# Performance work log

Measured on AMD Instinct MI355X. Metric: run time of the kernel, lower is better.

The kernel has to match this reference:

```python
import jax, jax.numpy as jnp
import numpy as np

DIM = 384; HEADS = 12; WS = 7; SHIFT = 3
IMG_H = 56; IMG_W = 56; B = 32; MLP_HID = 1536
N = WS * WS; HEAD_DIM = DIM // HEADS


def _rel_pos_index():
    # standard Swin relative position index, shape [N, N], values in [0, (2*WS-1)^2)
    coords = np.stack(np.meshgrid(np.arange(WS), np.arange(WS), indexing='ij')).reshape(2, -1)
    rel = (coords[:, :, None] - coords[:, None, :]).transpose(1, 2, 0)
    rel[..., 0] += WS - 1
    rel[..., 1] += WS - 1
    rel[..., 0] *= 2 * WS - 1
    return jnp.asarray(rel.sum(-1))

REL_IDX = _rel_pos_index()


def _shift_mask():
    # Swin shifted-window attention mask: 0 within region, -100 across regions
    img = np.zeros((IMG_H, IMG_W))
    cnt = 0
    for hs in (slice(0, -WS), slice(-WS, -SHIFT), slice(-SHIFT, None)):
        for ws_ in (slice(0, -WS), slice(-WS, -SHIFT), slice(-SHIFT, None)):
            img[hs, ws_] = cnt
            cnt += 1
    mw = img.reshape(IMG_H // WS, WS, IMG_W // WS, WS).transpose(0, 2, 1, 3).reshape(-1, N)
    am = mw[:, None, :] - mw[:, :, None]
    return jnp.asarray(np.where(am != 0, -100.0, 0.0).astype(np.float32))


def setup_inputs() -> dict:
    key = jax.random.key(0)
    ks = jax.random.split(key, 8)
    rn = lambda k, s: jax.random.normal(k, s, jnp.float32) * 0.02
    return {
        'x': jax.random.normal(ks[0], (B, IMG_H * IMG_W, DIM), jnp.float32),
        'mask': _shift_mask(),
        'w_ln1': jnp.ones((DIM,), jnp.float32), 'b_ln1': jnp.zeros((DIM,), jnp.float32),
        'w_qkv': rn(ks[1], (3 * DIM, DIM)), 'b_qkv': jnp.zeros((3 * DIM,), jnp.float32),
        'rel_bias': rn(ks[2], ((2 * WS - 1) ** 2, HEADS)),
        'w_proj': rn(ks[3], (DIM, DIM)), 'b_proj': jnp.zeros((DIM,), jnp.float32),
        'w_ln2': jnp.ones((DIM,), jnp.float32), 'b_ln2': jnp.zeros((DIM,), jnp.float32),
        'w_fc1': rn(ks[4], (MLP_HID, DIM)), 'b_fc1': jnp.zeros((MLP_HID,), jnp.float32),
        'w_fc2': rn(ks[5], (DIM, MLP_HID)), 'b_fc2': jnp.zeros((DIM,), jnp.float32),
        'H': IMG_H, 'W': IMG_W,
    }


def _ln(x, g, b, eps=1e-5):
    mu = x.mean(-1, keepdims=True)
    var = ((x - mu) ** 2).mean(-1, keepdims=True)
    return (x - mu) * jax.lax.rsqrt(var + eps) * g + b


def reference(x, mask, w_ln1, b_ln1, w_qkv, b_qkv, rel_bias, w_proj, b_proj,
              w_ln2, b_ln2, w_fc1, b_fc1, w_fc2, b_fc2, H, W):
    Bsz, L, C = x.shape
    nW = (H // WS) * (W // WS)
    shortcut = x
    h = _ln(x, w_ln1, b_ln1).reshape(Bsz, H, W, C)
    # cyclic shift
    h = jnp.roll(h, (-SHIFT, -SHIFT), axis=(1, 2))
    # window partition -> [B*nW, N, C]
    h = h.reshape(Bsz, H // WS, WS, W // WS, WS, C).transpose(0, 1, 3, 2, 4, 5).reshape(-1, N, C)
    nB = h.shape[0]
    qkv = (h @ w_qkv.T + b_qkv).reshape(nB, N, 3, HEADS, HEAD_DIM).transpose(2, 0, 3, 1, 4)
    q, k, v = qkv[0] * (HEAD_DIM ** -0.5), qkv[1], qkv[2]  # each [nB, heads, N, hd]
    attn = jnp.einsum('bhnd,bhmd->bhnm', q, k)
    bias = rel_bias[REL_IDX].transpose(2, 0, 1)  # [heads, N, N]
    attn = attn + bias[None]
    attn = attn.reshape(Bsz, nW, HEADS, N, N) + mask[None, :, None]
    attn = jax.nn.softmax(attn, axis=-1).reshape(nB, HEADS, N, N)
    o = jnp.einsum('bhnm,bhmd->bhnd', attn, v).transpose(0, 2, 1, 3).reshape(nB, N, C)
    o = o @ w_proj.T + b_proj
    # window reverse
    o = o.reshape(Bsz, H // WS, W // WS, WS, WS, C).transpose(0, 1, 3, 2, 4, 5).reshape(Bsz, H, W, C)
    o = jnp.roll(o, (SHIFT, SHIFT), axis=(1, 2)).reshape(Bsz, H * W, C)
    x = shortcut + o
    h2 = _ln(x, w_ln2, b_ln2)
    h2 = jax.nn.gelu(h2 @ w_fc1.T + b_fc1) @ w_fc2.T + b_fc2
    return x + h2
```

## Files before the change

### kernel.cpp

```cpp
#include <hip/hip_runtime.h>
#include <stdint.h>

#define B_     32
#define IMG    56
#define L_     (IMG*IMG)
#define C_     384
#define HEADS_ 12
#define HD     32
#define WS_    7
#define N_     49
#define NWIN   64
#define NB     (B_*NWIN)
#define M_TOK  (NB*N_)
#define QKVF   1152

typedef __attribute__((ext_vector_type(8))) short bf16x8;
typedef __attribute__((ext_vector_type(4))) float f32x4;
typedef __attribute__((ext_vector_type(4))) unsigned short u16x4;

__device__ __forceinline__ float bf2f(unsigned short u) {
  union { unsigned int u; float f; } c; c.u = ((unsigned int)u) << 16; return c.f;
}
__device__ __forceinline__ unsigned short f2bf(float f) {
  union { float f; unsigned int u; } c; c.f = f;
  unsigned int r = c.u + 0x7FFFu + ((c.u >> 16) & 1u);
  return (unsigned short)(r >> 16);
}

__device__ __forceinline__ void gload_lds16(const void* g, void* l) {
  __builtin_amdgcn_global_load_lds(
      (const __attribute__((address_space(1))) unsigned int*)(uintptr_t)g,
      (__attribute__((address_space(3))) unsigned int*)(uintptr_t)l,
      16, 0, 0);
}

#define MFMA16(a, b, c) __builtin_amdgcn_mfma_f32_16x16x32_bf16((a), (b), (c), 0, 0, 0)

__global__ __launch_bounds__(256) void k_prep(
    const float* __restrict__ w_qkv, const float* __restrict__ w_proj,
    const float* __restrict__ w_fc1, const float* __restrict__ w_fc2,
    const float* __restrict__ relb,  const float* __restrict__ mask,
    ushort* __restrict__ wbq, ushort* __restrict__ wbp,
    ushort* __restrict__ wb1, ushort* __restrict__ wb2,
    ushort* __restrict__ bm)
{
  int g = blockIdx.x * 256 + threadIdx.x;
  if (g < 442368)        { wbq[g]            = f2bf(w_qkv[g]); return; }
  if (g < 589824)        { wbp[g - 442368]   = f2bf(w_proj[g - 442368]); return; }
  if (g < 1179648)       { wb1[g - 589824]   = f2bf(w_fc1[g - 589824]); return; }
  if (g < 1769472)       { wb2[g - 1179648]  = f2bf(w_fc2[g - 1179648]); return; }
  int n = g - 1769472;
  int r    = n & 3;
  int col  = (n >> 2) & 63;
  int quad = (n >> 8) & 3;
  int i    = (n >> 10) & 3;
  int hw   = n >> 12;
  int h = hw % HEADS_, wc = hw / HEADS_;
  int row = i * 16 + quad * 4 + r;
  float v;
  if (col >= N_) v = -30000.f;
  else if (row >= N_) v = 0.f;
  else {
    int idx = (row / WS_ - col / WS_ + 6) * 13 + (row % WS_ - col % WS_ + 6);
    v = relb[idx * HEADS_ + h] + mask[((size_t)wc * N_ + row) * N_ + col];
  }
  bm[n] = f2bf(v);
}

template<bool WINDOW>
__global__ __launch_bounds__(256) void k_ln(const float* __restrict__ X,
    const float* __restrict__ G, const float* __restrict__ Bb,
    ushort* __restrict__ out)
{
  int token = blockIdx.x * 4 + (threadIdx.x >> 6);
  int lane  = threadIdx.x & 63;
  const float* xp = X + (size_t)token * C_;
  float v[6];
#pragma unroll
  for (int t = 0; t < 6; t++) v[t] = xp[lane + 64*t];
  float s = 0.f, s2 = 0.f;
#pragma unroll
  for (int t = 0; t < 6; t++) { s += v[t]; s2 += v[t]*v[t]; }
#pragma unroll
  for (int off = 32; off > 0; off >>= 1) {
    s  += __shfl_down(s,  off, 64);
    s2 += __shfl_down(s2, off, 64);
  }
  s = __shfl(s, 0, 64); s2 = __shfl(s2, 0, 64);
  float mu   = s * (1.f / C_);
  float rstd = rsqrtf(s2 * (1.f / C_) - mu * mu + 1e-5f);
  size_t obase;
  if (WINDOW) {
    int b = token / L_, pix = token % L_;
    int hi = pix / IMG, wj = pix % IMG;
    int sh = hi - 3; if (sh < 0) sh += IMG;
    int sw = wj - 3; if (sw < 0) sw += IMG;
    int w = b * NWIN + (sh / WS_) * 8 + (sw / WS_);
    int p = (sh % WS_) * WS_ + (sw % WS_);
    obase = ((size_t)w * N_ + p) * C_;
  } else {
    obase = (size_t)token * C_;
  }
#pragma unroll
  for (int t = 0; t < 6; t++) {
    int c = lane + 64*t;
    out[obase + c] = f2bf((v[t] - mu) * rstd * G[c] + Bb[c]);
  }
}

template<int EPI, typename OutT>
__global__ __launch_bounds__(256, 2) void k_gemm(
    const ushort* __restrict__ A, const ushort* __restrict__ W,
    const float* __restrict__ bias, OutT* __restrict__ out,
    const float* __restrict__ res, int M, int N, int K)
{
  __shared__ __align__(16) ushort As[2][256*32];
  __shared__ __align__(16) ushort Bs[2][128*32];
  int ntn = N >> 7;
  int nwg = gridDim.x;
  int bid = (blockIdx.x & 7) * (nwg >> 3) + (blockIdx.x >> 3);
  int m0 = (bid / ntn) << 8;
  int n0 = (bid % ntn) << 7;
  int tid  = threadIdx.x;
  int wave = tid >> 6, lane = tid & 63;
  int l15  = lane & 15, quad = lane >> 4;
  int wm = (wave >> 1) << 7;
  int wn = (wave & 1) << 6;

  int srow = tid >> 2;
  int scol = (tid & 3) * 8;
  const ushort* gA = A + (size_t)(m0 + srow) * K + scol;
  const ushort* gB = W + (size_t)(n0 + srow) * K + scol;
  int oA = srow * 32 + scol;

  f32x4 acc[8][4];
#pragma unroll
  for (int i = 0; i < 8; i++)
#pragma unroll
    for (int j = 0; j < 4; j++) acc[i][j] = (f32x4){0.f, 0.f, 0.f, 0.f};

#pragma unroll
  for (int it = 0; it < 4; it++)
    gload_lds16(gA + (size_t)it * 64 * K, &As[0][oA + it * 2048]);
#pragma unroll
  for (int it = 0; it < 2; it++)
    gload_lds16(gB + (size_t)it * 64 * K, &Bs[0][oA + it * 2048]);
  gA += 32; gB += 32;
  asm volatile("s_waitcnt vmcnt(0)" : : : "memory");
  __syncthreads();

  int nt = K >> 5;
  int cur = 0;
  for (int t = 0; t < nt; t++) {
    int nxt = cur ^ 1;
    if (t + 1 < nt) {
#pragma unroll
      for (int it = 0; it < 4; it++)
        gload_lds16(gA + (size_t)it * 64 * K, &As[nxt][oA + it * 2048]);
#pragma unroll
      for (int it = 0; it < 2; it++)
        gload_lds16(gB + (size_t)it * 64 * K, &Bs[nxt][oA + it * 2048]);
      gA += 32; gB += 32;
    }
    bf16x8 af[8], bfr[4];
#pragma unroll
    for (int i = 0; i < 8; i++) af[i]  = *(const bf16x8*)&As[cur][(wm + i*16 + l15)*32 + quad*8];
#pragma unroll
    for (int j = 0; j < 4; j++) bfr[j] = *(const bf16x8*)&Bs[cur][(wn + j*16 + l15)*32 + quad*8];
#pragma unroll
    for (int i = 0; i < 8; i++)
#pragma unroll
      for (int j = 0; j < 4; j++)
        acc[i][j] = MFMA16(af[i], bfr[j], acc[i][j]);
    asm volatile("s_waitcnt vmcnt(0)" : : : "memory");
    __syncthreads();
    cur = nxt;
  }

  float bv[4];
#pragma unroll
  for (int j = 0; j < 4; j++) bv[j] = bias[n0 + wn + j*16 + l15];
#pragma unroll
  for (int i = 0; i < 8; i++) {
#pragma unroll
    for (int r = 0; r < 4; r++) {
      int row = m0 + wm + i*16 + quad*4 + r;
      size_t dstbase;
      if (EPI == 1) {
        int w = row / N_, p = row % N_;
        int b = w >> 6, wi = w & 63;
        int hi = (wi >> 3) * WS_ + p / WS_ + 3; if (hi >= IMG) hi -= IMG;
        int wj = (wi & 7)  * WS_ + p % WS_ + 3; if (wj >= IMG) wj -= IMG;
        dstbase = ((size_t)b * L_ + hi * IMG + wj) * C_;
      } else {
        dstbase = (size_t)row * N;
      }
#pragma unroll
      for (int j = 0; j < 4; j++) {
        int col = n0 + wn + j*16 + l15;
        float v = acc[i][j][r] + bv[j];
        if (EPI == 2) {
          float e = __expf(-1.5957691216057308f * (v + 0.044715f * v * v * v));
          v = v * __builtin_amdgcn_rcpf(1.f + e);
        }
        size_t dst = dstbase + col;
        if (EPI == 1) v += res[dst];
        if (EPI == 3) v += res[(size_t)row * N + col];
        if constexpr (sizeof(OutT) == 4) out[dst] = v;
        else                             out[dst] = f2bf(v);
      }
    }
  }
}

__global__ __launch_bounds__(256, 3) void k_attn_mfma(
    const ushort* __restrict__ qkv, const ushort* __restrict__ bm,
    ushort* __restrict__ out)
{
  __shared__ __align__(16) ushort Ps[4][64*64];
  __shared__ __align__(16) ushort Vt[4][32*64];
  int wave = threadIdx.x >> 6, lane = threadIdx.x & 63;
  int task = blockIdx.x * 4 + wave;
  int w = task / HEADS_, h = task % HEADS_;
  int l15 = lane & 15, quad = lane >> 4;

  const ushort* base = qkv + (size_t)w * N_ * QKVF + h * HD;

  bf16x8 qf[4], kf[4];
#pragma unroll
  for (int i = 0; i < 4; i++) {
    int rr = i * 16 + l15; if (rr > 48) rr = 48;
    const ushort* rp = base + (size_t)rr * QKVF + quad * 8;
    qf[i] = *(const bf16x8*)rp;
    kf[i] = *(const bf16x8*)(rp + C_);
  }

  {
    int m = lane > 48 ? 48 : lane;
    const ushort* vp = base + (size_t)m * QKVF + 2 * C_;
    bf16x8 v0 = *(const bf16x8*)vp;
    bf16x8 v1 = *(const bf16x8*)(vp + 8);
    bf16x8 v2 = *(const bf16x8*)(vp + 16);
    bf16x8 v3 = *(const bf16x8*)(vp + 24);
    ushort* vt = &Vt[wave][0];
#pragma unroll
    for (int d = 0; d < 32; d++) {
      ushort val = (ushort)(d < 8 ? v0[d & 7] : d < 16 ? v1[d & 7]
                                  : d < 24 ? v2[d & 7] : v3[d & 7]);
      vt[d * 64 + (lane ^ ((d & 7) << 3))] = val;
    }
  }

  f32x4 acc[4][4];
#pragma unroll
  for (int i = 0; i < 4; i++)
#pragma unroll
    for (int j = 0; j < 4; j++) acc[i][j] = (f32x4){0.f, 0.f, 0.f, 0.f};
#pragma unroll
  for (int i = 0; i < 4; i++)
#pragma unroll
    for (int j = 0; j < 4; j++)
      acc[i][j] = MFMA16(qf[i], kf[j], acc[i][j]);

  const ushort* bmb = bm + ((size_t)(w & 63) * HEADS_ + h) * 4096;
  float sv[4][4][4];
#pragma unroll
  for (int i = 0; i < 4; i++)
#pragma unroll
    for (int j = 0; j < 4; j++) {
      u16x4 bv = *(const u16x4*)(bmb + (((i * 4 + quad) * 64) + (j * 16 + l15)) * 4);
#pragma unroll
      for (int r = 0; r < 4; r++)
        sv[i][j][r] = acc[i][j][r] * 0.17677669529663687f + bf2f(bv[r]);
    }

  float mx[4][4], sm[4][4];
#pragma unroll
  for (int i = 0; i < 4; i++)
#pragma unroll
    for (int r = 0; r < 4; r++)
      mx[i][r] = fmaxf(fmaxf(sv[i][0][r], sv[i][1][r]),
                       fmaxf(sv[i][2][r], sv[i][3][r]));
#pragma unroll
  for (int off = 1; off <= 8; off <<= 1)
#pragma unroll
    for (int i = 0; i < 4; i++)
#pragma unroll
      for (int r = 0; r < 4; r++)
        mx[i][r] = fmaxf(mx[i][r], __shfl_xor(mx[i][r], off, 64));
#pragma unroll
  for (int i = 0; i < 4; i++)
#pragma unroll
    for (int r = 0; r < 4; r++) sm[i][r] = 0.f;
#pragma unroll
  for (int i = 0; i < 4; i++)
#pragma unroll
    for (int j = 0; j < 4; j++)
#pragma unroll
      for (int r = 0; r < 4; r++) {
        float e = __expf(sv[i][j][r] - mx[i][r]);
        sv[i][j][r] = e;
        sm[i][r] += e;
      }
#pragma unroll
  for (int off = 1; off <= 8; off <<= 1)
#pragma unroll
    for (int i = 0; i < 4; i++)
#pragma unroll
      for (int r = 0; r < 4; r++)
        sm[i][r] += __shfl_xor(sm[i][r], off, 64);

  ushort* pw = &Ps[wave][0];
#pragma unroll
  for (int i = 0; i < 4; i++)
#pragma unroll
    for (int r = 0; r < 4; r++) {
      float inv = __builtin_amdgcn_rcpf(sm[i][r]);
      int row = i * 16 + quad * 4 + r;
      int s = (row & 7) << 3;
#pragma unroll
      for (int j = 0; j < 4; j++)
        pw[row * 64 + ((j * 16 + l15) ^ s)] = f2bf(sv[i][j][r] * inv);
    }

  f32x4 o[4][2];
#pragma unroll
  for (int i = 0; i < 4; i++)
#pragma unroll
    for (int jv = 0; jv < 2; jv++) o[i][jv] = (f32x4){0.f, 0.f, 0.f, 0.f};
  const ushort* vt = &Vt[wave][0];
#pragma unroll
  for (int ks = 0; ks < 2; ks++) {
    int kc = ks * 32 + quad * 8;
    bf16x8 pa[4], vb[2];
#pragma unroll
    for (int i = 0; i < 4; i++) {
      int row = i * 16 + l15;
      pa[i] = *(const bf16x8*)&pw[row * 64 + (kc ^ ((row & 7) << 3))];
    }
#pragma unroll
    for (int jv = 0; jv < 2; jv++) {
      int nn = jv * 16 + l15;
      vb[jv] = *(const bf16x8*)&vt[nn * 64 + (kc ^ ((nn & 7) << 3))];
    }
#pragma unroll
    for (int i = 0; i < 4; i++)
#pragma unroll
      for (int jv = 0; jv < 2; jv++)
        o[i][jv] = MFMA16(pa[i], vb[jv], o[i][jv]);
  }

  ushort* op = out + ((size_t)w * N_) * C_ + h * HD;
#pragma unroll
  for (int i = 0; i < 4; i++)
#pragma unroll
    for (int r = 0; r < 4; r++) {
      int row = i * 16 + quad * 4 + r;
      if (row < N_) {
#pragma unroll
        for (int jv = 0; jv < 2; jv++)
          op[(size_t)row * C_ + jv * 16 + l15] = f2bf(o[i][jv][r]);
      }
    }
}

extern "C" void kernel_launch(void* const* d_in, const int* in_sizes, int n_in,
                              void* d_out, int out_size, void* d_ws, size_t ws_size,
                              hipStream_t stream) {
  (void)in_sizes; (void)n_in; (void)out_size; (void)ws_size;
  const float* x      = (const float*)d_in[0];
  const float* mask   = (const float*)d_in[1];
  const float* w_ln1  = (const float*)d_in[2];
  const float* b_ln1  = (const float*)d_in[3];
  const float* w_qkv  = (const float*)d_in[4];
  const float* b_qkv  = (const float*)d_in[5];
  const float* relb   = (const float*)d_in[6];
  const float* w_proj = (const float*)d_in[7];
  const float* b_proj = (const float*)d_in[8];
  const float* w_ln2  = (const float*)d_in[9];
  const float* b_ln2  = (const float*)d_in[10];
  const float* w_fc1  = (const float*)d_in[11];
  const float* b_fc1  = (const float*)d_in[12];
  const float* w_fc2  = (const float*)d_in[13];
  const float* b_fc2  = (const float*)d_in[14];

  char* ws = (char*)d_ws;
  ushort* r0 = (ushort*)ws;
  ushort* r1 = (ushort*)(ws + 308281344);
  ushort* bmt = (ushort*)(ws + 231211008);
  ushort* wbq = (ushort*)(ws + 385351680);
  ushort* wbp = wbq + QKVF * C_;
  ushort* wb1 = wbp + C_ * C_;
  ushort* wb2 = wb1 + 1536 * C_;
  float*  x1   = (float*)d_out;
  float*  outp = (float*)d_out;

  k_prep<<<4915200/256, 256, 0, stream>>>(w_qkv, w_proj, w_fc1, w_fc2,
                                          relb, mask, wbq, wbp, wb1, wb2, bmt);

  k_ln<true ><<<M_TOK/4, 256, 0, stream>>>(x, w_ln1, b_ln1, r1);
  k_gemm<0, ushort><<<(M_TOK/256)*(QKVF/128), 256, 0, stream>>>(
      r1, wbq, b_qkv, r0, nullptr, M_TOK, QKVF, 384);
  k_attn_mfma<<<NB*HEADS_/4, 256, 0, stream>>>(r0, bmt, r1);
  k_gemm<1, float><<<(M_TOK/256)*(C_/128), 256, 0, stream>>>(
      r1, wbp, b_proj, x1, x, M_TOK, C_, 384);
  k_ln<false><<<M_TOK/4, 256, 0, stream>>>(x1, w_ln2, b_ln2, r1);
  k_gemm<2, ushort><<<(M_TOK/256)*(1536/128), 256, 0, stream>>>(
      r1, wb1, b_fc1, r0, nullptr, M_TOK, 1536, 384);
  k_gemm<3, float><<<(M_TOK/256)*(C_/128), 256, 0, stream>>>(
      r0, wb2, b_fc2, outp, x1, M_TOK, C_, 1536);
}
```

Measured before the change: 1.004 ms.

## Rewrite GEMM as 8-wave kernel with triple-buffered BK=64 LDS pipeline

Replaces the 4-wave double-buffered GEMM with an 8-wave (512-thread) kernel. Each wave now owns a 64x64 tile, and the kernel uses K-tiles of 64 with three LDS stages. The A/B tiles are stored in XOR-swizzled LDS to avoid bank conflicts. Global-to-LDS prefetch is split across two half-iterations, and the MFMA blocks run under raised s_setprio with partial vmcnt waits, so loads overlap compute. LDS use grows to 144KB per block, which limits occupancy to one block per CU, and the barrier-heavy schedule must be correct for every K.

Result: slower. 1.054 ms (+5.0%).

```diff
diff --git a/kernel.cpp b/kernel.cpp
--- a/kernel.cpp
+++ b/kernel.cpp
@@ -109,13 +109,13 @@
 }
 
 template<int EPI, typename OutT>
-__global__ __launch_bounds__(256, 2) void k_gemm(
+__global__ __launch_bounds__(512) void k_gemm8(
     const ushort* __restrict__ A, const ushort* __restrict__ W,
     const float* __restrict__ bias, OutT* __restrict__ out,
     const float* __restrict__ res, int M, int N, int K)
 {
-  __shared__ __align__(16) ushort As[2][256*32];
-  __shared__ __align__(16) ushort Bs[2][128*32];
+  __shared__ __align__(16) ushort As[3][256*64];
+  __shared__ __align__(16) ushort Bs[3][128*64];
   int ntn = N >> 7;
   int nwg = gridDim.x;
   int bid = (blockIdx.x & 7) * (nwg >> 3) + (blockIdx.x >> 3);
@@ -124,64 +124,101 @@
   int tid  = threadIdx.x;
   int wave = tid >> 6, lane = tid & 63;
   int l15  = lane & 15, quad = lane >> 4;
-  int wm = (wave >> 1) << 7;
+  int wm = (wave >> 1) << 6;
   int wn = (wave & 1) << 6;
 
-  int srow = tid >> 2;
-  int scol = (tid & 3) * 8;
-  const ushort* gA = A + (size_t)(m0 + srow) * K + scol;
-  const ushort* gB = W + (size_t)(n0 + srow) * K + scol;
-  int oA = srow * 32 + scol;
-
-  f32x4 acc[8][4];
-#pragma unroll
-  for (int i = 0; i < 8; i++)
+  int srow = (wave << 3) + (lane >> 3);
+  int lgsw = (lane & 7) ^ ((lane >> 3) & 7);
+  const ushort* gAs = A + (size_t)(m0 + srow) * K + lgsw * 8;
+  const ushort* gBs = W + (size_t)(n0 + srow) * K + lgsw * 8;
+  int oL = (wave << 9) + (lane << 3);
+
+  int pg0 = quad ^ (l15 & 7);
+
+  f32x4 acc[4][4];
+#pragma unroll
+  for (int i = 0; i < 4; i++)
 #pragma unroll
     for (int j = 0; j < 4; j++) acc[i][j] = (f32x4){0.f, 0.f, 0.f, 0.f};
 
 #pragma unroll
-  for (int it = 0; it < 4; it++)
-    gload_lds16(gA + (size_t)it * 64 * K, &As[0][oA + it * 2048]);
-#pragma unroll
-  for (int it = 0; it < 2; it++)
-    gload_lds16(gB + (size_t)it * 64 * K, &Bs[0][oA + it * 2048]);
-  gA += 32; gB += 32;
-  asm volatile("s_waitcnt vmcnt(0)" : : : "memory");
-  __syncthreads();
-
-  int nt = K >> 5;
-  int cur = 0;
+  for (int tt = 0; tt < 2; tt++) {
+#pragma unroll
+    for (int ro = 0; ro < 4; ro++)
+      gload_lds16(gAs + (size_t)(ro * 64) * K + tt * 64, &As[tt][ro * 4096 + oL]);
+#pragma unroll
+    for (int ro = 0; ro < 2; ro++)
+      gload_lds16(gBs + (size_t)(ro * 64) * K + tt * 64, &Bs[tt][ro * 4096 + oL]);
+  }
+  asm volatile("s_waitcnt vmcnt(6)" ::: "memory");
+  __builtin_amdgcn_s_barrier();
+
+  int nt = K >> 6;
+  int rd = 0, wr = 2;
+  int kcol = 128;
   for (int t = 0; t < nt; t++) {
-    int nxt = cur ^ 1;
-    if (t + 1 < nt) {
-#pragma unroll
-      for (int it = 0; it < 4; it++)
-        gload_lds16(gA + (size_t)it * 64 * K, &As[nxt][oA + it * 2048]);
-#pragma unroll
-      for (int it = 0; it < 2; it++)
-        gload_lds16(gB + (size_t)it * 64 * K, &Bs[nxt][oA + it * 2048]);
-      gA += 32; gB += 32;
-    }
-    bf16x8 af[8], bfr[4];
-#pragma unroll
-    for (int i = 0; i < 8; i++) af[i]  = *(const bf16x8*)&As[cur][(wm + i*16 + l15)*32 + quad*8];
-#pragma unroll
-    for (int j = 0; j < 4; j++) bfr[j] = *(const bf16x8*)&Bs[cur][(wn + j*16 + l15)*32 + quad*8];
-#pragma unroll
-    for (int i = 0; i < 8; i++)
+    bool pre = (t + 2 < nt);
+    const ushort* as = &As[0][0] + rd * 16384;
+    const ushort* bs = &Bs[0][0] + rd * 8192;
+
+    bf16x8 af[4], bfr[4];
+#pragma unroll
+    for (int i = 0; i < 4; i++)
+      af[i]  = *(const bf16x8*)&as[(wm + i*16 + l15) * 64 + pg0 * 8];
+#pragma unroll
+    for (int j = 0; j < 4; j++)
+      bfr[j] = *(const bf16x8*)&bs[(wn + j*16 + l15) * 64 + pg0 * 8];
+    if (pre) {
+#pragma unroll
+      for (int ro = 0; ro < 3; ro++)
+        gload_lds16(gAs + (size_t)(ro * 64) * K + kcol, &As[wr][ro * 4096 + oL]);
+    }
+    __builtin_amdgcn_s_barrier();
+    __builtin_amdgcn_s_setprio(1);
+#pragma unroll
+    for (int i = 0; i < 4; i++)
 #pragma unroll
       for (int j = 0; j < 4; j++)
         acc[i][j] = MFMA16(af[i], bfr[j], acc[i][j]);
-    asm volatile("s_waitcnt vmcnt(0)" : : : "memory");
-    __syncthreads();
-    cur = nxt;
+    __builtin_amdgcn_s_setprio(0);
+    __builtin_amdgcn_s_barrier();
+
+#pragma unroll
+    for (int i = 0; i < 4; i++)
+      af[i]  = *(const bf16x8*)&as[(wm + i*16 + l15) * 64 + (pg0 ^ 4) * 8];
+#pragma unroll
+    for (int j = 0; j < 4; j++)
+      bfr[j] = *(const bf16x8*)&bs[(wn + j*16 + l15) * 64 + (pg0 ^ 4) * 8];
+    if (pre) {
+      gload_lds16(gAs + (size_t)(3 * 64) * K + kcol, &As[wr][3 * 4096 + oL]);
+#pragma unroll
+      for (int ro = 0; ro < 2; ro++)
+        gload_lds16(gBs + (size_t)(ro * 64) * K + kcol, &Bs[wr][ro * 4096 + oL]);
+      kcol += 64;
+    }
+    __builtin_amdgcn_s_barrier();
+    __builtin_amdgcn_s_setprio(1);
+#pragma unroll
+    for (int i = 0; i < 4; i++)
+#pragma unroll
+      for (int j = 0; j < 4; j++)
+        acc[i][j] = MFMA16(af[i], bfr[j], acc[i][j]);
+    __builtin_amdgcn_s_setprio(0);
+
+    if (t + 1 < nt) {
+      if (pre) asm volatile("s_waitcnt vmcnt(6)" ::: "memory");
+      else     asm volatile("s_waitcnt vmcnt(0)" ::: "memory");
+    }
+    __builtin_amdgcn_s_barrier();
+    rd = (rd == 2) ? 0 : rd + 1;
+    wr = (wr == 2) ? 0 : wr + 1;
   }
 
   float bv[4];
 #pragma unroll
   for (int j = 0; j < 4; j++) bv[j] = bias[n0 + wn + j*16 + l15];
 #pragma unroll
-  for (int i = 0; i < 8; i++) {
+  for (int i = 0; i < 4; i++) {
 #pragma unroll
     for (int r = 0; r < 4; r++) {
       int row = m0 + wm + i*16 + quad*4 + r;
@@ -399,14 +436,14 @@
                                           relb, mask, wbq, wbp, wb1, wb2, bmt);
 
   k_ln<true ><<<M_TOK/4, 256, 0, stream>>>(x, w_ln1, b_ln1, r1);
-  k_gemm<0, ushort><<<(M_TOK/256)*(QKVF/128), 256, 0, stream>>>(
+  k_gemm8<0, ushort><<<(M_TOK/256)*(QKVF/128), 512, 0, stream>>>(
       r1, wbq, b_qkv, r0, nullptr, M_TOK, QKVF, 384);
   k_attn_mfma<<<NB*HEADS_/4, 256, 0, stream>>>(r0, bmt, r1);
-  k_gemm<1, float><<<(M_TOK/256)*(C_/128), 256, 0, stream>>>(
+  k_gemm8<1, float><<<(M_TOK/256)*(C_/128), 512, 0, stream>>>(
       r1, wbp, b_proj, x1, x, M_TOK, C_, 384);
   k_ln<false><<<M_TOK/4, 256, 0, stream>>>(x1, w_ln2, b_ln2, r1);
-  k_gemm<2, ushort><<<(M_TOK/256)*(1536/128), 256, 0, stream>>>(
+  k_gemm8<2, ushort><<<(M_TOK/256)*(1536/128), 512, 0, stream>>>(
       r1, wb1, b_fc1, r0, nullptr, M_TOK, 1536, 384);
-  k_gemm<3, float><<<(M_TOK/256)*(C_/128), 256, 0, stream>>>(
+  k_gemm8<3, float><<<(M_TOK/256)*(C_/128), 512, 0, stream>>>(
       r0, wb2, b_fc2, outp, x1, M_TOK, C_, 1536);
 }
```
